# Optimization experiments

Hardware: AMD Instinct MI355X
Metric: run time of the kernel (lower is better)

## Reference

```python
import jax, jax.numpy as jnp
import numpy as np

D_MODEL = 1024
NUM_HEADS = 16
HEAD_DIM = D_MODEL // NUM_HEADS
B, L = 4, 4096


def _linear(x, w, b):
    # torch nn.Linear: y = x @ w.T + b, w: [out, in]
    return jnp.einsum('bld,od->blo', x, w) + b


def _elu_feature_map(x):
    return jax.nn.elu(x) + 1.0


def setup_inputs() -> dict:
    key = jax.random.key(0)
    ks = jax.random.split(key, 11)
    s = 1.0 / np.sqrt(D_MODEL)
    inp = {
        'query': jax.random.normal(ks[0], (B, L, D_MODEL), jnp.float32),
        'key': jax.random.normal(ks[1], (B, L, D_MODEL), jnp.float32),
        'value': jax.random.normal(ks[2], (B, L, D_MODEL), jnp.float32),
        'wq': jax.random.uniform(ks[3], (D_MODEL, D_MODEL), jnp.float32, -s, s),
        'bq': jax.random.uniform(ks[4], (D_MODEL,), jnp.float32, -s, s),
        'wk': jax.random.uniform(ks[5], (D_MODEL, D_MODEL), jnp.float32, -s, s),
        'bk': jax.random.uniform(ks[6], (D_MODEL,), jnp.float32, -s, s),
        'wv': jax.random.uniform(ks[7], (D_MODEL, D_MODEL), jnp.float32, -s, s),
        'bv': jax.random.uniform(ks[8], (D_MODEL,), jnp.float32, -s, s),
        'wo': jax.random.uniform(ks[9], (D_MODEL, D_MODEL), jnp.float32, -s, s),
        'bo': jax.random.uniform(ks[10], (D_MODEL,), jnp.float32, -s, s),
    }
    return inp


def reference(query, key, value, wq, bq, wk, bk, wv, bv, wo, bo):
    Bsz, Lq, _ = query.shape
    # project and split heads -> [B, H, L, hd]
    def split_heads(x):
        return x.reshape(Bsz, -1, NUM_HEADS, HEAD_DIM).transpose(0, 2, 1, 3)
    Q = split_heads(_linear(query, wq, bq))
    K = split_heads(_linear(key, wk, bk))
    V = split_heads(_linear(value, wv, bv))
    Q = _elu_feature_map(Q)
    K = _elu_feature_map(K)
    # KV: [B, H, hd, hd]
    KV = jnp.einsum('bhld,bhle->bhde', K, V)
    Ksum = K.sum(axis=2)  # [B, H, hd]
    Z = 1.0 / (jnp.einsum('bhld,bhd->bhl', Q, Ksum) + 1e-6)  # [B, H, Lq]
    out = jnp.einsum('bhld,bhde->bhle', Q, KV) * Z[..., None]
    out = out.transpose(0, 2, 1, 3).reshape(Bsz, Lq, D_MODEL)
    return _linear(out, wo, bo)
```

## Files before the change

kernel.cpp:

```cpp
#include <hip/hip_runtime.h>
#include <hip/hip_bf16.h>

typedef _Float16 half8 __attribute__((ext_vector_type(8)));
typedef _Float16 half4 __attribute__((ext_vector_type(4)));
typedef float f32x4 __attribute__((ext_vector_type(4)));

#define KDIM 1024
#define NDIM 1024
#define MROWS 16384

#define GLD_LDS16(g, l)                                                  \
  __builtin_amdgcn_global_load_lds(                                      \
      (const __attribute__((address_space(1))) void*)(g),                \
      (__attribute__((address_space(3))) void*)(l), 16, 0, 0)

__global__ __launch_bounds__(256)
void cvt_f32_to_f16(const float* __restrict__ src, _Float16* __restrict__ dst,
                    int n8) {
  for (int i = blockIdx.x * 256 + threadIdx.x; i < n8; i += gridDim.x * 256) {
    float4 f0 = ((const float4*)src)[2 * i];
    float4 f1 = ((const float4*)src)[2 * i + 1];
    half8 h;
    h[0] = (_Float16)f0.x; h[1] = (_Float16)f0.y;
    h[2] = (_Float16)f0.z; h[3] = (_Float16)f0.w;
    h[4] = (_Float16)f1.x; h[5] = (_Float16)f1.y;
    h[6] = (_Float16)f1.z; h[7] = (_Float16)f1.w;
    ((half8*)dst)[i] = h;
  }
}

template <int ACT, int TRANS, int FUSE, typename TOUT>
__global__ __launch_bounds__(512, 2)
void gemm_big(const _Float16* __restrict__ X, const _Float16* __restrict__ W,
              const float* __restrict__ bias, TOUT* __restrict__ Y,
              const _Float16* __restrict__ KVTx) {
  constexpr int BM = 256, BN = 128, BK = 64;
  __shared__ _Float16 As[3 * BM * BK];
  __shared__ _Float16 Bs[3 * BN * BK];

  const int tid  = threadIdx.x;
  const int lane = tid & 63;
  const int w    = tid >> 6;
  const int wm   = w >> 1;
  const int wn   = w & 1;

  const int bid = blockIdx.x;
  const int wid = (bid & 7) * 64 + (bid >> 3);
  const int m0  = (wid >> 3) * BM;
  const int n0  = (wid & 7) * BN;

  const int lr = lane >> 3;
  const int ls = (lane & 7) ^ lr;

#define STAGE_TILE(kt, bidx)                                                  \
  {                                                                           \
    const int k0s = (kt) * BK;                                                \
    _Float16* la = As + (bidx) * (BM * BK) + w * 512;                         \
    _Float16* lb = Bs + (bidx) * (BN * BK) + w * 512;                         \
    _Pragma("unroll")                                                         \
    for (int j = 0; j < 4; ++j)                                               \
      GLD_LDS16(X + (size_t)(m0 + w * 8 + 64 * j + lr) * KDIM + k0s + ls * 8, \
                la + 4096 * j);                                               \
    _Pragma("unroll")                                                         \
    for (int j = 0; j < 2; ++j)                                               \
      GLD_LDS16(W + (size_t)(n0 + w * 8 + 64 * j + lr) * KDIM + k0s + ls * 8, \
                lb + 4096 * j);                                               \
  }

  f32x4 acc[4][4] = {};

  STAGE_TILE(0, 0);
  STAGE_TILE(1, 1);
  asm volatile("s_waitcnt vmcnt(6)" ::: "memory");
  asm volatile("s_barrier" ::: "memory");

  int bc = 0;
  for (int t = 0; t < 16; ++t) {
    int bs = bc + 2; if (bs >= 3) bs -= 3;
    const char* Ab = (const char*)As + bc * (BM * BK * 2);
    const char* Bb = (const char*)Bs + bc * (BN * BK * 2);

    half8 afr[4][2], bfr[4][2];
#pragma unroll
    for (int mi = 0; mi < 4; ++mi)
#pragma unroll
      for (int kk = 0; kk < 2; ++kk) {
        int row  = wm * 64 + mi * 16 + (lane & 15);
        int byte = row * 128 + ((lane >> 4) << 4) + kk * 64;
        byte ^= (row & 7) << 4;
        afr[mi][kk] = *(const half8*)(Ab + byte);
      }
#pragma unroll
    for (int ni = 0; ni < 4; ++ni)
#pragma unroll
      for (int kk = 0; kk < 2; ++kk) {
        int row  = wn * 64 + ni * 16 + (lane & 15);
        int byte = row * 128 + ((lane >> 4) << 4) + kk * 64;
        byte ^= (row & 7) << 4;
        bfr[ni][kk] = *(const half8*)(Bb + byte);
      }

    if (t < 14) STAGE_TILE(t + 2, bs);

    __builtin_amdgcn_s_setprio(1);
#pragma unroll
    for (int kk = 0; kk < 2; ++kk)
#pragma unroll
      for (int mi = 0; mi < 4; ++mi)
#pragma unroll
        for (int ni = 0; ni < 4; ++ni)
          acc[mi][ni] = __builtin_amdgcn_mfma_f32_16x16x32_f16(
              afr[mi][kk], bfr[ni][kk], acc[mi][ni], 0, 0, 0);
    __builtin_amdgcn_s_setprio(0);

    if (t < 14) {
      asm volatile("s_waitcnt vmcnt(6)" ::: "memory");
      asm volatile("s_barrier" ::: "memory");
    } else if (t == 14) {
      asm volatile("s_waitcnt vmcnt(0)" ::: "memory");
      asm volatile("s_barrier" ::: "memory");
    }
    ++bc; if (bc == 3) bc = 0;
  }
#undef STAGE_TILE

  if constexpr (FUSE) {
    __syncthreads();
    _Float16* Ct = As;
#pragma unroll
    for (int ni = 0; ni < 4; ++ni) {
      int cl   = wn * 64 + ni * 16 + (lane & 15);
      float bv = bias[n0 + cl];
#pragma unroll
      for (int mi = 0; mi < 4; ++mi) {
#pragma unroll
        for (int i = 0; i < 4; ++i) {
          int row = wm * 64 + mi * 16 + ((lane >> 4) << 2) + i;
          float v = acc[mi][ni][i] + bv;
          v = (v > 0.f) ? (v + 1.f) : __expf(v);
          int byte = row * 256 + cl * 2;
          byte ^= (row & 7) << 4;
          *(_Float16*)((char*)Ct + byte) = (_Float16)v;
        }
      }
    }
    _Float16* KVs = Bs;
    const int bh0 = ((m0 >> 12) << 4) + (n0 >> 6);
    for (int c = tid; c < 1280; c += 512) {
      int hh  = (c >= 640) ? 1 : 0;
      int cc  = c - hh * 640;
      int row = cc >> 3;
      int co8 = (cc & 7) << 3;
      int byte = hh * 10240 + row * 128 + co8 * 2;
      byte ^= (row & 7) << 4;
      *(half8*)((char*)KVs + byte) =
          *(const half8*)(KVTx + (size_t)(bh0 + hh) * 5120 + cc * 8);
    }
    __syncthreads();
    f32x4 acc2[4][5] = {};
#pragma unroll
    for (int kk = 0; kk < 2; ++kk) {
      half8 afr2[4], bfr2[5];
#pragma unroll
      for (int m = 0; m < 4; ++m) {
        int row  = wm * 64 + m * 16 + (lane & 15);
        int byte = row * 256 + wn * 128 + kk * 64 + ((lane >> 4) << 4);
        byte ^= (row & 7) << 4;
        afr2[m] = *(const half8*)((const char*)Ct + byte);
      }
#pragma unroll
      for (int n = 0; n < 5; ++n) {
        int row  = n * 16 + (lane & 15);
        int byte = wn * 10240 + row * 128 + kk * 64 + ((lane >> 4) << 4);
        byte ^= (row & 7) << 4;
        bfr2[n] = *(const half8*)((const char*)KVs + byte);
      }
#pragma unroll
      for (int m = 0; m < 4; ++m)
#pragma unroll
        for (int n = 0; n < 5; ++n)
          acc2[m][n] = __builtin_amdgcn_mfma_f32_16x16x32_f16(
              afr2[m], bfr2[n], acc2[m][n], 0, 0, 0);
    }
#pragma unroll
    for (int m = 0; m < 4; ++m) {
#pragma unroll
      for (int i = 0; i < 4; ++i) {
        float dn = __shfl(acc2[m][4][i], lane & 48);
        float z  = 1.f / (dn + 1e-6f);
        size_t row = (size_t)m0 + wm * 64 + m * 16 + ((lane >> 4) << 2) + i;
#pragma unroll
        for (int n = 0; n < 4; ++n) {
          int col = n0 + wn * 64 + n * 16 + (lane & 15);
          Y[row * NDIM + col] = (TOUT)(acc2[m][n][i] * z);
        }
      }
    }
    return;
  }

#pragma unroll
  for (int ni = 0; ni < 4; ++ni) {
    int col  = n0 + wn * 64 + ni * 16 + (lane & 15);
    float bv = bias[col];
#pragma unroll
    for (int mi = 0; mi < 4; ++mi) {
      int r0 = m0 + wm * 64 + mi * 16 + ((lane >> 4) << 2);
      if constexpr (TRANS) {
        int b  = r0 >> 12;
        int l0 = r0 & 4095;
        half4 hv;
#pragma unroll
        for (int i = 0; i < 4; ++i) {
          float v = acc[mi][ni][i] + bv;
          if constexpr (ACT == 1) v = (v > 0.f) ? (v + 1.f) : __expf(v);
          hv[i] = (_Float16)v;
        }
        *(half4*)((_Float16*)Y + ((size_t)(b * 1024 + col)) * 4096 + l0) = hv;
      } else {
#pragma unroll
        for (int i = 0; i < 4; ++i) {
          float v = acc[mi][ni][i] + bv;
          if constexpr (ACT == 1) v = (v > 0.f) ? (v + 1.f) : __expf(v);
          Y[(size_t)(r0 + i) * NDIM + col] = (TOUT)v;
        }
      }
    }
  }
}

__global__ __launch_bounds__(256, 2)
void kv_mfma(const _Float16* __restrict__ KT, const _Float16* __restrict__ VT,
             _Float16* __restrict__ pKV) {
  const int bh = blockIdx.x;
  const int ch = blockIdx.y;
  const int tid  = threadIdx.x;
  const int lane = tid & 63;
  const int w    = tid >> 6;

  __shared__ _Float16 As[64 * 64];
  __shared__ _Float16 Bs[64 * 64];

  const int lr = lane >> 3;
  const int ls = (lane & 7) ^ lr;
  const size_t lbase = (size_t)ch * 512 + ls * 8;
  const _Float16* gA = VT + (size_t)(bh * 64 + w * 16 + lr) * 4096 + lbase;
  const _Float16* gB = KT + (size_t)(bh * 64 + w * 16 + lr) * 4096 + lbase;
  _Float16* ldsA = As + (w * 16) * 64;
  _Float16* ldsB = Bs + (w * 16) * 64;

  half8 aones;
#pragma unroll
  for (int j = 0; j < 8; ++j) aones[j] = (lane & 15) == 0 ? (_Float16)1.0f : (_Float16)0.0f;

  f32x4 acc[5] = {};

  for (int k0 = 0; k0 < 512; k0 += 64) {
    __syncthreads();
#pragma unroll
    for (int c = 0; c < 2; ++c) {
      GLD_LDS16(gA + k0 + (size_t)(c * 8) * 4096, ldsA + c * 8 * 64);
      GLD_LDS16(gB + k0 + (size_t)(c * 8) * 4096, ldsB + c * 8 * 64);
    }
    __syncthreads();

    half8 afr[4][2], bfr[2];
#pragma unroll
    for (int m = 0; m < 4; ++m)
#pragma unroll
      for (int kk = 0; kk < 2; ++kk) {
        int row  = m * 16 + (lane & 15);
        int byte = row * 128 + ((lane >> 4) << 4) + kk * 64;
        byte ^= (row & 7) << 4;
        afr[m][kk] = *(const half8*)((const char*)As + byte);
      }
#pragma unroll
    for (int kk = 0; kk < 2; ++kk) {
      int row  = w * 16 + (lane & 15);
      int byte = row * 128 + ((lane >> 4) << 4) + kk * 64;
      byte ^= (row & 7) << 4;
      bfr[kk] = *(const half8*)((const char*)Bs + byte);
    }
#pragma unroll
    for (int kk = 0; kk < 2; ++kk) {
#pragma unroll
      for (int m = 0; m < 4; ++m)
        acc[m] = __builtin_amdgcn_mfma_f32_16x16x32_f16(afr[m][kk], bfr[kk],
                                                        acc[m], 0, 0, 0);
      acc[4] = __builtin_amdgcn_mfma_f32_16x16x32_f16(aones, bfr[kk],
                                                      acc[4], 0, 0, 0);
    }
  }

  _Float16* outp = pKV + ((size_t)ch * 64 + bh) * 5120;
  const int col = w * 16 + (lane & 15);
#pragma unroll
  for (int m = 0; m < 5; ++m) {
#pragma unroll
    for (int i = 0; i < 4; ++i) {
      int row = m * 16 + ((lane >> 4) << 2) + i;
      outp[row * 64 + col] = (_Float16)acc[m][i];
    }
  }
}

__global__ __launch_bounds__(256)
void kv_combine(const _Float16* __restrict__ pKV, _Float16* __restrict__ KVTx) {
  int g = blockIdx.x * 256 + threadIdx.x;
  int bh = g / 5120;
  int j  = g - bh * 5120;
  float s = 0.f;
#pragma unroll
  for (int ch = 0; ch < 8; ++ch)
    s += (float)pKV[((size_t)ch * 64 + bh) * 5120 + j];
  KVTx[(size_t)bh * 5120 + j] = (_Float16)s;
}

extern "C" void kernel_launch(void* const* d_in, const int* in_sizes, int n_in,
                              void* d_out, int out_size, void* d_ws, size_t ws_size,
                              hipStream_t stream) {
  const float* q  = (const float*)d_in[0];
  const float* k  = (const float*)d_in[1];
  const float* v  = (const float*)d_in[2];
  const float* wq = (const float*)d_in[3];
  const float* bq = (const float*)d_in[4];
  const float* wk = (const float*)d_in[5];
  const float* bk = (const float*)d_in[6];
  const float* wv = (const float*)d_in[7];
  const float* bv = (const float*)d_in[8];
  const float* wo = (const float*)d_in[9];
  const float* bo = (const float*)d_in[10];
  float* out = (float*)d_out;

  char* ws = (char*)d_ws;
  _Float16* KT   = (_Float16*)(ws + 33554432);
  _Float16* VT   = (_Float16*)(ws + 67108864);
  _Float16* Wh   = (_Float16*)(ws + 100663296);
  _Float16* pKVh = (_Float16*)(ws + 102760448);
  _Float16* KVTx = (_Float16*)(ws + 108003328);
  _Float16* att  = KT;
  _Float16* Xh   = (_Float16*)d_out;

  const int N8_BIG = MROWS * KDIM / 8;
  const int N8_W   = KDIM * KDIM / 8;

  const int GBLK = (MROWS / 256) * (NDIM / 128);

  cvt_f32_to_f16<<<2048, 256, 0, stream>>>(k, Xh, N8_BIG);
  cvt_f32_to_f16<<<512, 256, 0, stream>>>(wk, Wh, N8_W);
  gemm_big<1, 1, 0, _Float16><<<GBLK, 512, 0, stream>>>(Xh, Wh, bk, KT, nullptr);
  cvt_f32_to_f16<<<2048, 256, 0, stream>>>(v, Xh, N8_BIG);
  cvt_f32_to_f16<<<512, 256, 0, stream>>>(wv, Wh, N8_W);
  gemm_big<0, 1, 0, _Float16><<<GBLK, 512, 0, stream>>>(Xh, Wh, bv, VT, nullptr);

  kv_mfma<<<dim3(64, 8), 256, 0, stream>>>(KT, VT, pKVh);
  kv_combine<<<1280, 256, 0, stream>>>(pKVh, KVTx);

  cvt_f32_to_f16<<<2048, 256, 0, stream>>>(q, Xh, N8_BIG);
  cvt_f32_to_f16<<<512, 256, 0, stream>>>(wq, Wh, N8_W);
  gemm_big<1, 0, 1, _Float16><<<GBLK, 512, 0, stream>>>(Xh, Wh, bq, att, KVTx);

  cvt_f32_to_f16<<<512, 256, 0, stream>>>(wo, Wh, N8_W);
  gemm_big<0, 0, 0, float><<<GBLK, 512, 0, stream>>>(att, Wh, bo, out, nullptr);
}
```

Baseline: 263.8 us.

## Halve GEMM K-tile to fit two blocks per CU and batch conversions

Drops the GEMM K-tile from 64 to 32 with a new swizzle, cutting LDS per block from roughly 144 KB to 72 KB so two 512-thread blocks can co-reside on a CU. All four weight conversions and all three activation conversions are merged into two launches with one conversion buffer per tensor. The workspace is rearranged so buffers are reused once they are dead. The KV reduction split drops from 8 to 4 chunks, and the fused Q epilogue reads KV fragments straight from global memory instead of staging them in LDS. The cost is twice as many barrier-synchronised K iterations, each doing less MFMA work, plus uncoalesced global fragment loads in the epilogue.

```diff
diff --git a/kernel.cpp b/kernel.cpp
--- a/kernel.cpp
+++ b/kernel.cpp
@@ -15,28 +15,45 @@
       (__attribute__((address_space(3))) void*)(l), 16, 0, 0)
 
 __global__ __launch_bounds__(256)
-void cvt_f32_to_f16(const float* __restrict__ src, _Float16* __restrict__ dst,
-                    int n8) {
-  for (int i = blockIdx.x * 256 + threadIdx.x; i < n8; i += gridDim.x * 256) {
-    float4 f0 = ((const float4*)src)[2 * i];
-    float4 f1 = ((const float4*)src)[2 * i + 1];
+void cvt32(const float* __restrict__ s0, _Float16* __restrict__ d0,
+           const float* __restrict__ s1, _Float16* __restrict__ d1,
+           const float* __restrict__ s2, _Float16* __restrict__ d2,
+           const float* __restrict__ s3, _Float16* __restrict__ d3) {
+  const float* src;
+  _Float16* dst;
+  switch (blockIdx.y) {
+    case 0: src = s0; dst = d0; break;
+    case 1: src = s1; dst = d1; break;
+    case 2: src = s2; dst = d2; break;
+    default: src = s3; dst = d3; break;
+  }
+  const size_t g = (size_t)blockIdx.x * 8192;
+  const int tid = threadIdx.x;
+  float4 f[8];
+#pragma unroll
+  for (int j = 0; j < 8; ++j)
+    f[j] = *(const float4*)(src + g + j * 1024 + tid * 4);
+#pragma unroll
+  for (int j = 0; j < 4; ++j) {
     half8 h;
-    h[0] = (_Float16)f0.x; h[1] = (_Float16)f0.y;
-    h[2] = (_Float16)f0.z; h[3] = (_Float16)f0.w;
-    h[4] = (_Float16)f1.x; h[5] = (_Float16)f1.y;
-    h[6] = (_Float16)f1.z; h[7] = (_Float16)f1.w;
-    ((half8*)dst)[i] = h;
+    h[0] = (_Float16)f[2 * j].x;     h[1] = (_Float16)f[2 * j].y;
+    h[2] = (_Float16)f[2 * j].z;     h[3] = (_Float16)f[2 * j].w;
+    h[4] = (_Float16)f[2 * j + 1].x; h[5] = (_Float16)f[2 * j + 1].y;
+    h[6] = (_Float16)f[2 * j + 1].z; h[7] = (_Float16)f[2 * j + 1].w;
+    *(half4*)(dst + g + 2 * j * 1024 + tid * 4) = half4{h[0], h[1], h[2], h[3]};
+    *(half4*)(dst + g + (2 * j + 1) * 1024 + tid * 4) = half4{h[4], h[5], h[6], h[7]};
   }
 }
 
 template <int ACT, int TRANS, int FUSE, typename TOUT>
 __global__ __launch_bounds__(512, 2)
-void gemm_big(const _Float16* __restrict__ X, const _Float16* __restrict__ W,
-              const float* __restrict__ bias, TOUT* __restrict__ Y,
-              const _Float16* __restrict__ KVTx) {
-  constexpr int BM = 256, BN = 128, BK = 64;
-  __shared__ _Float16 As[3 * BM * BK];
-  __shared__ _Float16 Bs[3 * BN * BK];
+void gemm_bk32(const _Float16* __restrict__ X, const _Float16* __restrict__ W,
+               const float* __restrict__ bias, TOUT* __restrict__ Y,
+               const _Float16* __restrict__ KVTx) {
+  constexpr int BM = 256, BN = 128, BK = 32;
+  __shared__ char smem[73728];
+  _Float16* As = (_Float16*)smem;
+  _Float16* Bs = (_Float16*)(smem + 49152);
 
   const int tid  = threadIdx.x;
   const int lane = tid & 63;
@@ -49,84 +66,73 @@
   const int m0  = (wid >> 3) * BM;
   const int n0  = (wid & 7) * BN;
 
-  const int lr = lane >> 3;
-  const int ls = (lane & 7) ^ lr;
-
-#define STAGE_TILE(kt, bidx)                                                  \
+  const int lrw = lane >> 2;
+  const int gsl = (lane & 3) ^ (lrw & 3);
+  const _Float16* gA = X + (size_t)(m0 + w * 16 + lrw) * KDIM + gsl * 8;
+  const _Float16* gB = W + (size_t)(n0 + w * 16 + lrw) * KDIM + gsl * 8;
+
+#define STAGE32(kt, bidx)                                                     \
   {                                                                           \
     const int k0s = (kt) * BK;                                                \
-    _Float16* la = As + (bidx) * (BM * BK) + w * 512;                         \
-    _Float16* lb = Bs + (bidx) * (BN * BK) + w * 512;                         \
-    _Pragma("unroll")                                                         \
-    for (int j = 0; j < 4; ++j)                                               \
-      GLD_LDS16(X + (size_t)(m0 + w * 8 + 64 * j + lr) * KDIM + k0s + ls * 8, \
-                la + 4096 * j);                                               \
-    _Pragma("unroll")                                                         \
-    for (int j = 0; j < 2; ++j)                                               \
-      GLD_LDS16(W + (size_t)(n0 + w * 8 + 64 * j + lr) * KDIM + k0s + ls * 8, \
-                lb + 4096 * j);                                               \
-  }
+    _Float16* la = As + (bidx) * (BM * BK) + (w * 16) * BK;                   \
+    _Float16* lb = Bs + (bidx) * (BN * BK) + (w * 16) * BK;                   \
+    GLD_LDS16(gA + k0s, la);                                                  \
+    GLD_LDS16(gA + (size_t)128 * KDIM + k0s, la + 128 * BK);                  \
+    GLD_LDS16(gB + k0s, lb);                                                  \
+  }
+
+  const int rsl = ((lane >> 4) ^ (lane & 3)) << 4;
 
   f32x4 acc[4][4] = {};
 
-  STAGE_TILE(0, 0);
-  STAGE_TILE(1, 1);
-  asm volatile("s_waitcnt vmcnt(6)" ::: "memory");
+  STAGE32(0, 0);
+  STAGE32(1, 1);
+  asm volatile("s_waitcnt vmcnt(3)" ::: "memory");
   asm volatile("s_barrier" ::: "memory");
 
   int bc = 0;
-  for (int t = 0; t < 16; ++t) {
+  for (int t = 0; t < 32; ++t) {
     int bs = bc + 2; if (bs >= 3) bs -= 3;
     const char* Ab = (const char*)As + bc * (BM * BK * 2);
     const char* Bb = (const char*)Bs + bc * (BN * BK * 2);
 
-    half8 afr[4][2], bfr[4][2];
+    half8 afr[4], bfr[4];
+#pragma unroll
+    for (int mi = 0; mi < 4; ++mi) {
+      int row = wm * 64 + mi * 16 + (lane & 15);
+      afr[mi] = *(const half8*)(Ab + row * 64 + rsl);
+    }
+#pragma unroll
+    for (int ni = 0; ni < 4; ++ni) {
+      int row = wn * 64 + ni * 16 + (lane & 15);
+      bfr[ni] = *(const half8*)(Bb + row * 64 + rsl);
+    }
+
+    if (t < 30) STAGE32(t + 2, bs);
+
+    __builtin_amdgcn_s_setprio(1);
 #pragma unroll
     for (int mi = 0; mi < 4; ++mi)
 #pragma unroll
-      for (int kk = 0; kk < 2; ++kk) {
-        int row  = wm * 64 + mi * 16 + (lane & 15);
-        int byte = row * 128 + ((lane >> 4) << 4) + kk * 64;
-        byte ^= (row & 7) << 4;
-        afr[mi][kk] = *(const half8*)(Ab + byte);
-      }
-#pragma unroll
-    for (int ni = 0; ni < 4; ++ni)
-#pragma unroll
-      for (int kk = 0; kk < 2; ++kk) {
-        int row  = wn * 64 + ni * 16 + (lane & 15);
-        int byte = row * 128 + ((lane >> 4) << 4) + kk * 64;
-        byte ^= (row & 7) << 4;
-        bfr[ni][kk] = *(const half8*)(Bb + byte);
-      }
-
-    if (t < 14) STAGE_TILE(t + 2, bs);
-
-    __builtin_amdgcn_s_setprio(1);
-#pragma unroll
-    for (int kk = 0; kk < 2; ++kk)
-#pragma unroll
-      for (int mi = 0; mi < 4; ++mi)
-#pragma unroll
-        for (int ni = 0; ni < 4; ++ni)
-          acc[mi][ni] = __builtin_amdgcn_mfma_f32_16x16x32_f16(
-              afr[mi][kk], bfr[ni][kk], acc[mi][ni], 0, 0, 0);
+      for (int ni = 0; ni < 4; ++ni)
+        acc[mi][ni] = __builtin_amdgcn_mfma_f32_16x16x32_f16(
+            afr[mi], bfr[ni], acc[mi][ni], 0, 0, 0);
     __builtin_amdgcn_s_setprio(0);
 
-    if (t < 14) {
-      asm volatile("s_waitcnt vmcnt(6)" ::: "memory");
+    if (t < 30) {
+      asm volatile("s_waitcnt vmcnt(3)" ::: "memory");
       asm volatile("s_barrier" ::: "memory");
-    } else if (t == 14) {
+    } else if (t == 30) {
       asm volatile("s_waitcnt vmcnt(0)" ::: "memory");
       asm volatile("s_barrier" ::: "memory");
     }
     ++bc; if (bc == 3) bc = 0;
   }
-#undef STAGE_TILE
+#undef STAGE32
 
   if constexpr (FUSE) {
     __syncthreads();
-    _Float16* Ct = As;
+    _Float16* Ct = (_Float16*)smem;
 #pragma unroll
     for (int ni = 0; ni < 4; ++ni) {
       int cl   = wn * 64 + ni * 16 + (lane & 15);
@@ -144,19 +150,9 @@
         }
       }
     }
-    _Float16* KVs = Bs;
+    __syncthreads();
     const int bh0 = ((m0 >> 12) << 4) + (n0 >> 6);
-    for (int c = tid; c < 1280; c += 512) {
-      int hh  = (c >= 640) ? 1 : 0;
-      int cc  = c - hh * 640;
-      int row = cc >> 3;
-      int co8 = (cc & 7) << 3;
-      int byte = hh * 10240 + row * 128 + co8 * 2;
-      byte ^= (row & 7) << 4;
-      *(half8*)((char*)KVs + byte) =
-          *(const half8*)(KVTx + (size_t)(bh0 + hh) * 5120 + cc * 8);
-    }
-    __syncthreads();
+    const _Float16* kvp = KVTx + (size_t)(bh0 + wn) * 5120;
     f32x4 acc2[4][5] = {};
 #pragma unroll
     for (int kk = 0; kk < 2; ++kk) {
@@ -170,10 +166,8 @@
       }
 #pragma unroll
       for (int n = 0; n < 5; ++n) {
-        int row  = n * 16 + (lane & 15);
-        int byte = wn * 10240 + row * 128 + kk * 64 + ((lane >> 4) << 4);
-        byte ^= (row & 7) << 4;
-        bfr2[n] = *(const half8*)((const char*)KVs + byte);
+        int row = n * 16 + (lane & 15);
+        bfr2[n] = *(const half8*)(kvp + row * 64 + kk * 32 + ((lane >> 4) << 3));
       }
 #pragma unroll
       for (int m = 0; m < 4; ++m)
@@ -243,7 +237,7 @@
 
   const int lr = lane >> 3;
   const int ls = (lane & 7) ^ lr;
-  const size_t lbase = (size_t)ch * 512 + ls * 8;
+  const size_t lbase = (size_t)ch * 1024 + ls * 8;
   const _Float16* gA = VT + (size_t)(bh * 64 + w * 16 + lr) * 4096 + lbase;
   const _Float16* gB = KT + (size_t)(bh * 64 + w * 16 + lr) * 4096 + lbase;
   _Float16* ldsA = As + (w * 16) * 64;
@@ -255,7 +249,7 @@
 
   f32x4 acc[5] = {};
 
-  for (int k0 = 0; k0 < 512; k0 += 64) {
+  for (int k0 = 0; k0 < 1024; k0 += 64) {
     __syncthreads();
 #pragma unroll
     for (int c = 0; c < 2; ++c) {
@@ -311,7 +305,7 @@
   int j  = g - bh * 5120;
   float s = 0.f;
 #pragma unroll
-  for (int ch = 0; ch < 8; ++ch)
+  for (int ch = 0; ch < 4; ++ch)
     s += (float)pKV[((size_t)ch * 64 + bh) * 5120 + j];
   KVTx[(size_t)bh * 5120 + j] = (_Float16)s;
 }
@@ -333,33 +327,31 @@
   float* out = (float*)d_out;
 
   char* ws = (char*)d_ws;
+  _Float16* Xq   = (_Float16*)(ws);
   _Float16* KT   = (_Float16*)(ws + 33554432);
   _Float16* VT   = (_Float16*)(ws + 67108864);
-  _Float16* Wh   = (_Float16*)(ws + 100663296);
-  _Float16* pKVh = (_Float16*)(ws + 102760448);
-  _Float16* KVTx = (_Float16*)(ws + 108003328);
+  _Float16* pKV  = (_Float16*)(ws + 100663296);
+  _Float16* whk  = (_Float16*)(ws + 100663296);
+  _Float16* whv  = (_Float16*)(ws + 102760448);
+  _Float16* whq  = (_Float16*)(ws + 104857600);
+  _Float16* who  = (_Float16*)(ws + 106954752);
   _Float16* att  = KT;
-  _Float16* Xh   = (_Float16*)d_out;
-
-  const int N8_BIG = MROWS * KDIM / 8;
-  const int N8_W   = KDIM * KDIM / 8;
+  _Float16* Xk   = (_Float16*)d_out;
+  _Float16* Xv   = (_Float16*)((char*)d_out + 33554432);
+  _Float16* KVTx = (_Float16*)((char*)d_out + 33554432);
 
   const int GBLK = (MROWS / 256) * (NDIM / 128);
 
-  cvt_f32_to_f16<<<2048, 256, 0, stream>>>(k, Xh, N8_BIG);
-  cvt_f32_to_f16<<<512, 256, 0, stream>>>(wk, Wh, N8_W);
-  gemm_big<1, 1, 0, _Float16><<<GBLK, 512, 0, stream>>>(Xh, Wh, bk, KT, nullptr);
-  cvt_f32_to_f16<<<2048, 256, 0, stream>>>(v, Xh, N8_BIG);
-  cvt_f32_to_f16<<<512, 256, 0, stream>>>(wv, Wh, N8_W);
-  gemm_big<0, 1, 0, _Float16><<<GBLK, 512, 0, stream>>>(Xh, Wh, bv, VT, nullptr);
-
-  kv_mfma<<<dim3(64, 8), 256, 0, stream>>>(KT, VT, pKVh);
-  kv_combine<<<1280, 256, 0, stream>>>(pKVh, KVTx);
-
-  cvt_f32_to_f16<<<2048, 256, 0, stream>>>(q, Xh, N8_BIG);
-  cvt_f32_to_f16<<<512, 256, 0, stream>>>(wq, Wh, N8_W);
-  gemm_big<1, 0, 1, _Float16><<<GBLK, 512, 0, stream>>>(Xh, Wh, bq, att, KVTx);
-
-  cvt_f32_to_f16<<<512, 256, 0, stream>>>(wo, Wh, N8_W);
-  gemm_big<0, 0, 0, float><<<GBLK, 512, 0, stream>>>(att, Wh, bo, out, nullptr);
-}
+  cvt32<<<dim3(128, 4), 256, 0, stream>>>(wq, whq, wk, whk, wv, whv, wo, who);
+  cvt32<<<dim3(2048, 3), 256, 0, stream>>>(k, Xk, v, Xv, q, Xq, nullptr, nullptr);
+
+  gemm_bk32<1, 1, 0, _Float16><<<GBLK, 512, 0, stream>>>(Xk, whk, bk, KT, nullptr);
+  gemm_bk32<0, 1, 0, _Float16><<<GBLK, 512, 0, stream>>>(Xv, whv, bv, VT, nullptr);
+
+  kv_mfma<<<dim3(64, 4), 256, 0, stream>>>(KT, VT, pKV);
+  kv_combine<<<1280, 256, 0, stream>>>(pKV, KVTx);
+
+  gemm_bk32<1, 0, 1, _Float16><<<GBLK, 512, 0, stream>>>(Xq, whq, bq, att, KVTx);
+
+  gemm_bk32<0, 0, 0, float><<<GBLK, 512, 0, stream>>>(att, who, bo, out, nullptr);
+}
```

Result: faster. 258.1 us (-2.2%).
